# Kernel optimization log

Hardware: AMD Instinct MI355X
Metric: run time of the kernel (lower is better)

The kernel has to match this reference:

```python
import math
import jax, jax.numpy as jnp
import numpy as np

D_MODEL = 1024
N_POLES = 32        # d_state // 2
DIRECTIONS = 2      # bidirectional
SEQ_LEN = 4096
DT_MIN, DT_MAX = 1e-3, 1e-1


def setup_inputs() -> dict:
    key = jax.random.key(0)
    k_dt, k_c = jax.random.split(key, 2)
    # log_dt ~ U[log(dt_min), log(dt_max)]
    log_dt = jax.random.uniform(k_dt, (D_MODEL,), dtype=jnp.float32) \
        * (math.log(DT_MAX) - math.log(DT_MIN)) + math.log(DT_MIN)
    # S4D-Lin initialization: real part -0.5, imag part pi*n
    log_a_real = jnp.log(0.5 * jnp.ones((D_MODEL, N_POLES), dtype=jnp.float32))
    a_imag = math.pi * jnp.tile(jnp.arange(N_POLES, dtype=jnp.float32)[None, :], (D_MODEL, 1))
    # complex coeffs stored as real view [..., 2]
    coeffs = jax.random.normal(k_c, (DIRECTIONS, D_MODEL, N_POLES, 2), dtype=jnp.float32)
    return {
        "log_dt": log_dt,
        "log_a_real": log_a_real,
        "a_imag": a_imag,
        "coeffs": coeffs,
        "sequence_length": SEQ_LEN,
    }


def reference(log_dt, log_a_real, a_imag, coeffs, sequence_length):
    dt = jnp.exp(log_dt)                                   # [H]
    c = coeffs[..., 0] + 1j * coeffs[..., 1]               # [dir, H, N] complex
    a = -jnp.exp(log_a_real) + 1j * a_imag                 # [H, N] complex
    timeline = jnp.arange(sequence_length, dtype=jnp.float32)  # [L]
    delta_a = a * dt[:, None]                              # [H, N]
    # Vandermonde matrix exp(delta_a * l): [H, N, L] complex (the big intermediate)
    vand = jnp.exp(delta_a[:, :, None] * timeline)
    scaled_c = c * (jnp.exp(delta_a) - 1.0) / a            # [dir, H, N]
    # contract over poles N -> [dir, H, L]
    kernels = 2.0 * jnp.real(jnp.einsum('dhn,hnl->dhl', scaled_c, vand))
    return kernels
```

## Files before the change

kernel.cpp:

```cpp
#include <hip/hip_runtime.h>
#include <math.h>


constexpr int H      = 1024;
constexpr int NP     = 32;
constexpr int L      = 4096;
constexpr int BLOCK  = 256;
constexpr int HALVES = 2;
constexpr int SEG    = L / HALVES;
constexpr int CHUNK  = SEG / BLOCK;

constexpr float  TWOPI    = 6.283185307179586f;
constexpr double INV2PI_D = 0.15915494309189535;

__global__ __launch_bounds__(BLOCK, 8)
void ssm_vand_kernel(const float* __restrict__ log_dt,
                     const float* __restrict__ log_a_real,
                     const float* __restrict__ a_imag,
                     const float* __restrict__ coeffs,
                     float* __restrict__ out)
{
    const int h    = blockIdx.x >> 1;
    const int half = blockIdx.x & 1;
    const int t    = threadIdx.x;

    __shared__ float4 pole[NP * 3];

    if (t < NP) {
        const int n = t;
        const float dtf = expf(log_dt[h]);
        const float ar  = -expf(log_a_real[h * NP + n]);
        const float ai  = a_imag[h * NP + n];
        const float dar = ar * dtf;
        const float dai = ai * dtf;

        const double rate  = (double)ai * (double)dtf * INV2PI_D;
        const double ratef = rate - floor(rate);
        const float  rhi   = (float)ratef;
        const float  rlo   = (float)(ratef - (double)rhi);

        const float e256 = expf(256.0f * dar);
        double r256 = 256.0 * rate;
        r256 -= floor(r256);
        float s256, c256;
        sincosf((float)r256 * TWOPI, &s256, &c256);

        const float ed = expf(dar);
        float sd, cd;
        sincosf(dai, &sd, &cd);
        const float emr = ed * cd - 1.0f;
        const float emi = ed * sd;
        const float inv = 1.0f / (ar * ar + ai * ai);
        const float gr  = (emr * ar + emi * ai) * inv;
        const float gi  = (emi * ar - emr * ai) * inv;

        const float cr0 = coeffs[((0 * H + h) * NP + n) * 2 + 0];
        const float ci0 = coeffs[((0 * H + h) * NP + n) * 2 + 1];
        const float cr1 = coeffs[((1 * H + h) * NP + n) * 2 + 0];
        const float ci1 = coeffs[((1 * H + h) * NP + n) * 2 + 1];

        pole[n * 3 + 0] = make_float4(dar, rhi, rlo, 0.0f);
        pole[n * 3 + 1] = make_float4(e256 * c256, e256 * s256, 0.0f, 0.0f);
        pole[n * 3 + 2] = make_float4(2.0f * (cr0 * gr - ci0 * gi),
                                      2.0f * (cr0 * gi + ci0 * gr),
                                      2.0f * (cr1 * gr - ci1 * gi),
                                      2.0f * (cr1 * gi + ci1 * gr));
    }
    __syncthreads();

    float acc0[CHUNK];
    float acc1[CHUNK];
    #pragma unroll
    for (int j = 0; j < CHUNK; ++j) { acc0[j] = 0.0f; acc1[j] = 0.0f; }

    const float lf = (float)(half * SEG + t);

    #pragma unroll 1
    for (int n = 0; n < NP; ++n) {
        const float4 pa = pole[n * 3 + 0];
        const float4 pz = pole[n * 3 + 1];
        const float4 ps = pole[n * 3 + 2];

        const float m = __expf(pa.x * lf);
        const float p = pa.y * lf;
        const float e = fmaf(pa.y, lf, -p);
        float rev = (p - floorf(p)) + fmaf(pa.z, lf, e);
        float s, c;
        __sincosf(rev * TWOPI, &s, &c);
        float wr = m * c;
        float wi = m * s;

        #pragma unroll
        for (int j = 0; j < CHUNK; ++j) {
            acc0[j] = fmaf(ps.x, wr, fmaf(-ps.y, wi, acc0[j]));
            acc1[j] = fmaf(ps.z, wr, fmaf(-ps.w, wi, acc1[j]));
            const float nwr = fmaf(wr, pz.x, -(wi * pz.y));
            wi              = fmaf(wi, pz.x,  (wr * pz.y));
            wr = nwr;
        }
    }

    float* o0 = out + (size_t)h * L + half * SEG + t;
    float* o1 = o0 + (size_t)H * L;
    #pragma unroll
    for (int j = 0; j < CHUNK; ++j) {
        o0[j * BLOCK] = acc0[j];
        o1[j * BLOCK] = acc1[j];
    }
}

extern "C" void kernel_launch(void* const* d_in, const int* in_sizes, int n_in,
                              void* d_out, int out_size, void* d_ws, size_t ws_size,
                              hipStream_t stream) {
    const float* log_dt     = (const float*)d_in[0];
    const float* log_a_real = (const float*)d_in[1];
    const float* a_imag     = (const float*)d_in[2];
    const float* coeffs     = (const float*)d_in[3];
    float* out = (float*)d_out;

    ssm_vand_kernel<<<dim3(H * HALVES), dim3(BLOCK), 0, stream>>>(
        log_dt, log_a_real, a_imag, coeffs, out);
}
```

Measured before the change: 98.07 us.

## Use real second-order recurrence for projected outputs and one block per channel

Replaces the complex rotation recurrence per step with a real two-term linear recurrence on the projected real parts (x_{j} = 2Re(z) x_{j-1} - |z|^2 x_{j-2}), which cuts per-step arithmetic roughly in half. Each block now covers the whole sequence of one channel (16 chunks per thread) instead of half of it, so the per-pole exp and sincos setup is amortized over more outputs. The low-order phase correction term is dropped. Risks are fewer blocks (1024) with higher register use, and reduced accuracy from the longer recurrence and the coarser phase.

Measured after the change: 93.50 us. 4.7% less time.

```diff
diff --git a/kernel.cpp b/kernel.cpp
--- a/kernel.cpp
+++ b/kernel.cpp
@@ -2,27 +2,24 @@
 #include <math.h>
 
 
-constexpr int H      = 1024;
-constexpr int NP     = 32;
-constexpr int L      = 4096;
-constexpr int BLOCK  = 256;
-constexpr int HALVES = 2;
-constexpr int SEG    = L / HALVES;
-constexpr int CHUNK  = SEG / BLOCK;
+constexpr int H     = 1024;
+constexpr int NP    = 32;
+constexpr int L     = 4096;
+constexpr int BLOCK = 256;
+constexpr int CHUNK = 16;
 
 constexpr float  TWOPI    = 6.283185307179586f;
 constexpr double INV2PI_D = 0.15915494309189535;
 
-__global__ __launch_bounds__(BLOCK, 8)
+__global__ __launch_bounds__(BLOCK, 4)
 void ssm_vand_kernel(const float* __restrict__ log_dt,
                      const float* __restrict__ log_a_real,
                      const float* __restrict__ a_imag,
                      const float* __restrict__ coeffs,
                      float* __restrict__ out)
 {
-    const int h    = blockIdx.x >> 1;
-    const int half = blockIdx.x & 1;
-    const int t    = threadIdx.x;
+    const int h = blockIdx.x;
+    const int t = threadIdx.x;
 
     __shared__ float4 pole[NP * 3];
 
@@ -35,15 +32,15 @@
         const float dai = ai * dtf;
 
         const double rate  = (double)ai * (double)dtf * INV2PI_D;
-        const double ratef = rate - floor(rate);
-        const float  rhi   = (float)ratef;
-        const float  rlo   = (float)(ratef - (double)rhi);
+        const float  rhi   = (float)(rate - floor(rate));
 
         const float e256 = expf(256.0f * dar);
         double r256 = 256.0 * rate;
         r256 -= floor(r256);
         float s256, c256;
         sincosf((float)r256 * TWOPI, &s256, &c256);
+        const float zr = e256 * c256;
+        const float zi = e256 * s256;
 
         const float ed = expf(dar);
         float sd, cd;
@@ -59,12 +56,14 @@
         const float cr1 = coeffs[((1 * H + h) * NP + n) * 2 + 0];
         const float ci1 = coeffs[((1 * H + h) * NP + n) * 2 + 1];
 
-        pole[n * 3 + 0] = make_float4(dar, rhi, rlo, 0.0f);
-        pole[n * 3 + 1] = make_float4(e256 * c256, e256 * s256, 0.0f, 0.0f);
-        pole[n * 3 + 2] = make_float4(2.0f * (cr0 * gr - ci0 * gi),
-                                      2.0f * (cr0 * gi + ci0 * gr),
-                                      2.0f * (cr1 * gr - ci1 * gi),
-                                      2.0f * (cr1 * gi + ci1 * gr));
+        pole[n * 3 + 0] = make_float4(dar, rhi, zr, zi);
+        pole[n * 3 + 1] = make_float4(2.0f * zr,
+                                      zr * zr + zi * zi,
+                                      2.0f * (cr0 * gr - ci0 * gi),
+                                      2.0f * (cr0 * gi + ci0 * gr));
+        pole[n * 3 + 2] = make_float4(2.0f * (cr1 * gr - ci1 * gi),
+                                      2.0f * (cr1 * gi + ci1 * gr),
+                                      0.0f, 0.0f);
     }
     __syncthreads();
 
@@ -73,34 +72,44 @@
     #pragma unroll
     for (int j = 0; j < CHUNK; ++j) { acc0[j] = 0.0f; acc1[j] = 0.0f; }
 
-    const float lf = (float)(half * SEG + t);
+    const float lf = (float)t;
 
     #pragma unroll 1
     for (int n = 0; n < NP; ++n) {
         const float4 pa = pole[n * 3 + 0];
-        const float4 pz = pole[n * 3 + 1];
-        const float4 ps = pole[n * 3 + 2];
+        const float4 pb = pole[n * 3 + 1];
+        const float4 pc = pole[n * 3 + 2];
 
         const float m = __expf(pa.x * lf);
-        const float p = pa.y * lf;
-        const float e = fmaf(pa.y, lf, -p);
-        float rev = (p - floorf(p)) + fmaf(pa.z, lf, e);
+        const float ph = pa.y * lf;
+        const float rev = ph - floorf(ph);
         float s, c;
         __sincosf(rev * TWOPI, &s, &c);
-        float wr = m * c;
-        float wi = m * s;
+        const float wr = m * c;
+        const float wi = m * s;
+        const float wr2 = fmaf(wr, pa.z, -(wi * pa.w));
+        const float wi2 = fmaf(wi, pa.z,  (wr * pa.w));
+
+        float x0p = fmaf(pb.z, wr,  -(pb.w * wi));
+        float x0  = fmaf(pb.z, wr2, -(pb.w * wi2));
+        float x1p = fmaf(pc.x, wr,  -(pc.y * wi));
+        float x1  = fmaf(pc.x, wr2, -(pc.y * wi2));
+
+        acc0[0] += x0p; acc1[0] += x1p;
+        acc0[1] += x0;  acc1[1] += x1;
 
         #pragma unroll
-        for (int j = 0; j < CHUNK; ++j) {
-            acc0[j] = fmaf(ps.x, wr, fmaf(-ps.y, wi, acc0[j]));
-            acc1[j] = fmaf(ps.z, wr, fmaf(-ps.w, wi, acc1[j]));
-            const float nwr = fmaf(wr, pz.x, -(wi * pz.y));
-            wi              = fmaf(wi, pz.x,  (wr * pz.y));
-            wr = nwr;
+        for (int j = 2; j < CHUNK; ++j) {
+            const float n0 = fmaf(pb.x, x0, -(pb.y * x0p));
+            const float n1 = fmaf(pb.x, x1, -(pb.y * x1p));
+            acc0[j] += n0;
+            acc1[j] += n1;
+            x0p = x0; x0 = n0;
+            x1p = x1; x1 = n1;
         }
     }
 
-    float* o0 = out + (size_t)h * L + half * SEG + t;
+    float* o0 = out + (size_t)h * L + t;
     float* o1 = o0 + (size_t)H * L;
     #pragma unroll
     for (int j = 0; j < CHUNK; ++j) {
@@ -118,6 +127,6 @@
     const float* coeffs     = (const float*)d_in[3];
     float* out = (float*)d_out;
 
-    ssm_vand_kernel<<<dim3(H * HALVES), dim3(BLOCK), 0, stream>>>(
+    ssm_vand_kernel<<<dim3(H), dim3(BLOCK), 0, stream>>>(
         log_dt, log_a_real, a_imag, coeffs, out);
 }
```
